# Performance work log

Hardware: AMD Instinct MI355X
Metric: run time of the kernel (lower is better)

## Reference

```python
import jax, jax.numpy as jnp
import numpy as np

B, C, Cs, CI, H, W = 4, 256, 256, 128, 64, 64

def setup_inputs() -> dict:
    key = jax.random.key(0)
    ks = jax.random.split(key, 9)
    sq = 1.0 / np.sqrt(C)
    ss = 1.0 / np.sqrt(Cs)
    return {
        "x_main": jax.random.normal(ks[0], (B, C, H, W), jnp.float32),
        "z_p": jax.random.normal(ks[1], (B, Cs, H, W), jnp.float32),
        "Wq": jax.random.normal(ks[2], (CI, C), jnp.float32) * sq,
        "bq": jax.random.normal(ks[3], (CI,), jnp.float32) * 0.01,
        "Wk": jax.random.normal(ks[4], (CI, Cs), jnp.float32) * ss,
        "bk": jax.random.normal(ks[5], (CI,), jnp.float32) * 0.01,
        "Wv": jax.random.normal(ks[6], (C, Cs), jnp.float32) * ss,
        "bv": jax.random.normal(ks[7], (C,), jnp.float32) * 0.01,
        "gamma": jax.random.normal(ks[8], (1,), jnp.float32) * 0.1,
    }

def reference(x_main, z_p, Wq, bq, Wk, bk, Wv, bv, gamma):
    b, c, h, w = x_main.shape
    n = h * w
    xm = x_main.reshape(b, c, n)          # [B, C, N]
    zf = z_p.reshape(b, z_p.shape[1], n)  # [B, Cs, M] (M == N here)
    # 1x1 convs == per-pixel channel projections
    q = jnp.einsum('oc,bcn->bon', Wq, xm) + bq[None, :, None]  # [B, CI, N]
    k = jnp.einsum('oc,bcm->bom', Wk, zf) + bk[None, :, None]  # [B, CI, M]
    v = jnp.einsum('oc,bcm->bom', Wv, zf) + bv[None, :, None]  # [B, C, M]
    # energy[b, n, m] = q_n . k_m  (no scaling, as in the original)
    energy = jnp.einsum('bcn,bcm->bnm', q, k)
    attention = jax.nn.softmax(energy, axis=-1)
    out = jnp.einsum('bom,bnm->bon', v, attention)  # [B, C, N]
    out = out.reshape(b, c, h, w)
    return gamma * out + x_main
```

## Files before the change

### kernel.cpp

```cpp
#include <hip/hip_runtime.h>
#include <hip/hip_bf16.h>


typedef __bf16  bf16x8  __attribute__((ext_vector_type(8)));
typedef float   f32x16  __attribute__((ext_vector_type(16)));

#define LOG2E 1.4426950408889634f

union BF8 { __hip_bfloat162 h[4]; bf16x8 v; };

__device__ inline bf16x8 pack8(const float f[8]) {
  BF8 u;
#pragma unroll
  for (int i = 0; i < 4; i++)
    u.h[i] = __float22bfloat162_rn(float2{f[2 * i], f[2 * i + 1]});
  return u.v;
}

__device__ inline void dma16(const void* g, void* l) {
  __builtin_amdgcn_global_load_lds(
      (const __attribute__((address_space(1))) unsigned int*)g,
      (__attribute__((address_space(3))) unsigned int*)l, 16, 0, 0);
}

__global__ __launch_bounds__(256, 2) void proj_mfma(
    const float* __restrict__ x, const float* __restrict__ z,
    const float* __restrict__ Wq, const float* __restrict__ bq,
    const float* __restrict__ Wk, const float* __restrict__ bk,
    const float* __restrict__ Wv, const float* __restrict__ bv,
    __hip_bfloat16* __restrict__ qp, __hip_bfloat16* __restrict__ kp,
    __hip_bfloat16* __restrict__ vp)
{
  extern __shared__ float xs[];
  const int bi = blockIdx.x;
  int mode, b, t, h = 0;
  if (bi < 512) { mode = bi >> 8; b = (bi & 255) >> 6; t = bi & 63; }
  else { int j = bi - 512; mode = 2; b = j >> 7; t = (j & 127) >> 1; h = j & 1; }
  const int n0 = t * 64;
  const float* X    = (mode == 0) ? x  : z;
  const float* W    = (mode == 0) ? Wq : (mode == 1) ? Wk : Wv;
  const float* bias = (mode == 0) ? bq : (mode == 1) ? bk : bv;

  const int tid = threadIdx.x;
  const int w = tid >> 6, lane = tid & 63, l32 = lane & 31, half = lane >> 5;

  {
    const float* gx = X + (size_t)b * (256 * 4096) + n0
                    + (size_t)(lane >> 4) * 4096 + (lane & 15) * 4;
#pragma unroll
    for (int it = 0; it < 16; it++) {
      int ch0 = w * 64 + it * 4;
      dma16(gx + (size_t)ch0 * 4096, xs + ch0 * 64 + lane * 4);
    }
  }

  const int obase = (mode == 2) ? 128 * h : 0;
  const int och = obase + w * 32 + l32;
  bf16x8 wf[16];
  {
    const float* wr = W + (size_t)och * 256 + half * 8;
#pragma unroll
    for (int cs = 0; cs < 16; cs++) {
      float f[8];
#pragma unroll
      for (int j = 0; j < 8; j++) f[j] = wr[cs * 16 + j];
      wf[cs] = pack8(f);
    }
  }
  __syncthreads();

  f32x16 O0, O1;
#pragma unroll
  for (int r = 0; r < 16; r++) { O0[r] = 0.f; O1[r] = 0.f; }

  const float* xc = xs + (half * 8) * 64 + l32;
  if (mode != 2) {
#pragma unroll
    for (int cs = 0; cs < 16; cs++) {
      float f0[8], f1[8];
#pragma unroll
      for (int j = 0; j < 8; j++) {
        f0[j] = xc[cs * 1024 + j * 64];
        f1[j] = xc[cs * 1024 + j * 64 + 32];
      }
      bf16x8 x0 = pack8(f0), x1 = pack8(f1);
      O0 = __builtin_amdgcn_mfma_f32_32x32x16_bf16(x0, wf[cs], O0, 0, 0, 0);
      O1 = __builtin_amdgcn_mfma_f32_32x32x16_bf16(x1, wf[cs], O1, 0, 0, 0);
    }
  } else {
#pragma unroll
    for (int cs = 0; cs < 16; cs++) {
      float f0[8], f1[8];
#pragma unroll
      for (int j = 0; j < 8; j++) {
        f0[j] = xc[cs * 1024 + j * 64];
        f1[j] = xc[cs * 1024 + j * 64 + 32];
      }
      bf16x8 x0 = pack8(f0), x1 = pack8(f1);
      O0 = __builtin_amdgcn_mfma_f32_32x32x16_bf16(wf[cs], x0, O0, 0, 0, 0);
      O1 = __builtin_amdgcn_mfma_f32_32x32x16_bf16(wf[cs], x1, O1, 0, 0, 0);
    }
  }

  if (mode == 0) {
    const float bb = bias[och];
    __hip_bfloat16* qb = qp + (size_t)(b * 4096 + n0) * 128 + och;
#pragma unroll
    for (int p = 0; p < 2; p++) {
      const f32x16& O = p ? O1 : O0;
#pragma unroll
      for (int r = 0; r < 16; r++) {
        int pix = p * 32 + (r & 3) + 8 * (r >> 2) + 4 * half;
        qb[(size_t)pix * 128] = __float2bfloat16((O[r] + bb) * LOG2E);
      }
    }
  } else if (mode == 1) {
    const float bb = bias[och];
    __hip_bfloat16* kb = kp + (size_t)(b * 128) * 4096
        + (och >> 4) * 512 + ((och >> 3) & 1) * 256 + (och & 7);
#pragma unroll
    for (int p = 0; p < 2; p++) {
      const f32x16& O = p ? O1 : O0;
#pragma unroll
      for (int r = 0; r < 16; r++) {
        int key = n0 + p * 32 + (r & 3) + 8 * (r >> 2) + 4 * half;
        kb[(size_t)(key >> 5) * 4096 + (key & 31) * 8] =
            __float2bfloat16(O[r] + bb);
      }
    }
  } else {
    float bvv[16];
#pragma unroll
    for (int r = 0; r < 16; r++)
      bvv[r] = bias[128 * h + 32 * w + (r & 3) + 8 * (r >> 2) + 4 * half];
    __hip_bfloat16* vb = vp + (size_t)(b * 128 + t * 2) * 8192
        + (4 * h + w) * 1024 + ((l32 >> 4) & 1) * 512 + ((l32 >> 3) & 1) * 256
        + (l32 & 7);
#pragma unroll
    for (int p = 0; p < 2; p++) {
      const f32x16& O = p ? O1 : O0;
#pragma unroll
      for (int r = 0; r < 16; r++) {
        int row = (r & 3) + 8 * (r >> 2) + 4 * half;
        vb[(size_t)p * 8192 + row * 8] = __float2bfloat16(O[r] + bvv[r]);
      }
    }
  }
}

struct AttnSmem {
  union {
    __hip_bfloat16 kbuf[2][8192];
    float ostage[256][33];
  } u;
  float redu[4][32];
  float rinv[32];
};

union U4 { unsigned u[4]; bf16x8 v; };

__global__ __launch_bounds__(256, 2) void attn_kernel(
    const __hip_bfloat16* __restrict__ qv, const __hip_bfloat16* __restrict__ kv,
    const __hip_bfloat16* __restrict__ vv,
    const float* __restrict__ x_main, const float* __restrict__ gammap,
    float* __restrict__ out)
{
  __shared__ AttnSmem sm;
  const int i  = blockIdx.x;
  const int b  = (i & 7) >> 1;
  const int qt = ((i >> 3) << 1) | (i & 1);
  const int n0 = qt * 32;
  const int tid  = threadIdx.x;
  const int w    = tid >> 6, lane = tid & 63, l32 = lane & 31, half = lane >> 5;
  const int kh   = w >> 1, chh = w & 1;

  bf16x8 qf[8];
  {
    const __hip_bfloat16* qb = qv + ((size_t)(b * 4096 + n0 + l32)) * 128 + half * 8;
#pragma unroll
    for (int cs = 0; cs < 8; cs++) qf[cs] = *(const bf16x8*)(qb + cs * 16);
  }

  const __hip_bfloat16* kg = kv + (size_t)(b * 128) * 4096;
  const __hip_bfloat16* vg = vv + (size_t)(b * 128) * 8192;

  auto stage = [&](int t) {
    __hip_bfloat16* kd = sm.u.kbuf[t & 1];
    const __hip_bfloat16* ksrc = kg + (size_t)t * 8192 + lane * 8;
#pragma unroll
    for (int c = 0; c < 4; c++) {
      int ck = w * 4 + c;
      dma16(ksrc + ck * 512, kd + ck * 512 + lane * 8);
    }
  };

  f32x16 Oacc[4];
#pragma unroll
  for (int c = 0; c < 4; c++)
#pragma unroll
    for (int r = 0; r < 16; r++) Oacc[c][r] = 0.f;

  float l_lane = 0.f;

  auto qk_tile = [&](int t) -> f32x16 {
    const __hip_bfloat16* kbase = sm.u.kbuf[t & 1] + kh * 4096 + lane * 8;
    f32x16 Sa, Sb;
#pragma unroll
    for (int r = 0; r < 16; r++) { Sa[r] = 0.f; Sb[r] = 0.f; }
#pragma unroll
    for (int cs = 0; cs < 4; cs++) {
      bf16x8 kf = *(const bf16x8*)(kbase + cs * 512);
      Sa = __builtin_amdgcn_mfma_f32_32x32x16_bf16(kf, qf[cs], Sa, 0, 0, 0);
    }
#pragma unroll
    for (int cs = 4; cs < 8; cs++) {
      bf16x8 kf = *(const bf16x8*)(kbase + cs * 512);
      Sb = __builtin_amdgcn_mfma_f32_32x32x16_bf16(kf, qf[cs], Sb, 0, 0, 0);
    }
    return Sa + Sb;
  };

  auto pv_tile = [&](int t, const f32x16& S) {
    unsigned p2[8];
    float lsub = 0.f;
#pragma unroll
    for (int t2 = 0; t2 < 8; t2++) {
      float a = exp2f(S[2 * t2]     - 64.0f);
      float c = exp2f(S[2 * t2 + 1] - 64.0f);
      lsub += a + c;
      union { __hip_bfloat162 h; unsigned u; } cv;
      cv.h = __float22bfloat162_rn(float2{a, c});
      p2[t2] = cv.u;
    }
    l_lane += lsub;
    unsigned r2[8];
#pragma unroll
    for (int t2 = 0; t2 < 8; t2++) r2[t2] = (unsigned)__shfl_xor((int)p2[t2], 32);
    U4 f0, f1;
    if (half == 0) {
      f0.u[0] = p2[0]; f0.u[1] = p2[1]; f0.u[2] = r2[0]; f0.u[3] = r2[1];
      f1.u[0] = p2[4]; f1.u[1] = p2[5]; f1.u[2] = r2[4]; f1.u[3] = r2[5];
    } else {
      f0.u[0] = r2[2]; f0.u[1] = r2[3]; f0.u[2] = p2[2]; f0.u[3] = p2[3];
      f1.u[0] = r2[6]; f1.u[1] = r2[7]; f1.u[2] = p2[6]; f1.u[3] = p2[7];
    }
    const bf16x8 pf0 = f0.v, pf1 = f1.v;
    const __hip_bfloat16* vb = vg + (size_t)(t * 2 + kh) * 8192
                             + chh * 4096 + lane * 8;
#pragma unroll
    for (int c = 0; c < 4; c++) {
      bf16x8 v0 = *(const bf16x8*)(vb + c * 1024);
      Oacc[c] = __builtin_amdgcn_mfma_f32_32x32x16_bf16(pf0, v0, Oacc[c], 0, 0, 0);
      bf16x8 v1 = *(const bf16x8*)(vb + c * 1024 + 512);
      Oacc[c] = __builtin_amdgcn_mfma_f32_32x32x16_bf16(pf1, v1, Oacc[c], 0, 0, 0);
    }
  };

  stage(0);
  __syncthreads();
  stage(1);
  {
    f32x16 S = qk_tile(0);
    pv_tile(0, S);
  }
#pragma unroll 1
  for (int t = 1; t < 64; ++t) {
    __syncthreads();
    if (t < 63) stage(t + 1);
    f32x16 S = qk_tile(t);
    pv_tile(t, S);
  }

  float lfull = l_lane + __shfl_xor(l_lane, 32);
  if (lane < 32) sm.redu[w][l32] = lfull;
  __syncthreads();
  if (kh == 0) {
#pragma unroll
    for (int c = 0; c < 4; c++) {
      int ch = (chh * 4 + c) * 32 + l32;
#pragma unroll
      for (int r = 0; r < 16; r++) {
        int q = (r & 3) + 8 * (r >> 2) + 4 * half;
        sm.u.ostage[ch][q] = Oacc[c][r];
      }
    }
  }
  if (tid < 32) sm.rinv[tid] = 1.0f / (sm.redu[0][tid] + sm.redu[2][tid]);
  __syncthreads();
  if (kh == 1) {
#pragma unroll
    for (int c = 0; c < 4; c++) {
      int ch = (chh * 4 + c) * 32 + l32;
#pragma unroll
      for (int r = 0; r < 16; r++) {
        int q = (r & 3) + 8 * (r >> 2) + 4 * half;
        sm.u.ostage[ch][q] += Oacc[c][r];
      }
    }
  }
  __syncthreads();

  const float gmm = gammap[0];
  const int pix = tid & 31;
  const float ri = sm.rinv[pix];
#pragma unroll
  for (int j = 0; j < 32; ++j) {
    int ch = (tid >> 5) * 32 + j;
    size_t g = ((size_t)(b * 256 + ch)) * 4096 + n0 + pix;
    out[g] = gmm * sm.u.ostage[ch][pix] * ri + x_main[g];
  }
}

extern "C" void kernel_launch(void* const* d_in, const int* in_sizes, int n_in,
                              void* d_out, int out_size, void* d_ws, size_t ws_size,
                              hipStream_t stream) {
  (void)in_sizes; (void)n_in; (void)out_size; (void)ws_size;
  const float* x  = (const float*)d_in[0];
  const float* z  = (const float*)d_in[1];
  const float* Wq = (const float*)d_in[2];
  const float* bq = (const float*)d_in[3];
  const float* Wk = (const float*)d_in[4];
  const float* bk = (const float*)d_in[5];
  const float* Wv = (const float*)d_in[6];
  const float* bv = (const float*)d_in[7];
  const float* gm = (const float*)d_in[8];
  float* out = (float*)d_out;

  char* ws = (char*)d_ws;
  const size_t QSZ = (size_t)4 * 4096 * 128 * sizeof(__hip_bfloat16);
  __hip_bfloat16* qp = (__hip_bfloat16*)(ws);
  __hip_bfloat16* kp = (__hip_bfloat16*)(ws + QSZ);
  __hip_bfloat16* vp = (__hip_bfloat16*)(ws + 2 * QSZ);

  const int proj_smem = 256 * 64 * sizeof(float);
  (void)hipFuncSetAttribute((const void*)proj_mfma,
                            hipFuncAttributeMaxDynamicSharedMemorySize,
                            proj_smem);

  proj_mfma<<<1024, 256, proj_smem, stream>>>(x, z, Wq, bq, Wk, bk, Wv, bv,
                                              qp, kp, vp);
  attn_kernel<<<512, 256, 0, stream>>>(qp, kp, vp, x, gm, out);
}
```

Before: 242.2 us.

## Pre-pack inputs and weights into MFMA fragment layout, drop attention shuffles

Adds a prep kernel that converts x, z and the three weight matrices to bf16 in MFMA-fragment-tiled layouts. The projection kernel then loads operands directly with vector loads and writes Q/K in a fragment layout, with a key permutation chosen so the attention kernel no longer needs cross-half shuffles to build P fragments. Attention also swaps operand order in PV, uses a single QK accumulator, and raises occupancy to 3 blocks. In exchange there is an extra kernel launch and an extra bf16 round trip of x and z through global memory.

```diff
diff --git a/kernel.cpp b/kernel.cpp
--- a/kernel.cpp
+++ b/kernel.cpp
@@ -8,6 +8,7 @@
 #define LOG2E 1.4426950408889634f
 
 union BF8 { __hip_bfloat162 h[4]; bf16x8 v; };
+union U4  { unsigned u[4]; bf16x8 v; };
 
 __device__ inline bf16x8 pack8(const float f[8]) {
   BF8 u;
@@ -23,126 +24,130 @@
       (__attribute__((address_space(3))) unsigned int*)l, 16, 0, 0);
 }
 
+__global__ __launch_bounds__(256) void prep_kernel(
+    const float* __restrict__ x, const float* __restrict__ z,
+    const float* __restrict__ Wq, const float* __restrict__ Wk,
+    const float* __restrict__ Wv,
+    __hip_bfloat16* __restrict__ xf, __hip_bfloat16* __restrict__ zf,
+    __hip_bfloat16* __restrict__ wfr)
+{
+  __shared__ float lds[256 * 65];
+  const int bi = blockIdx.x;
+  const int tid = threadIdx.x;
+  if (bi < 512) {
+    const int sel = bi >> 8;
+    const int b   = (bi >> 6) & 3;
+    const int pc  = bi & 63;
+    const float* in = sel ? z : x;
+    __hip_bfloat16* outp = sel ? zf : xf;
+    const size_t ib = (size_t)b * 256 * 4096 + pc * 64;
+#pragma unroll 4
+    for (int r = 0; r < 64; r++) {
+      int ch = r * 4 + (tid >> 6);
+      lds[ch * 65 + (tid & 63)] = in[ib + (size_t)ch * 4096 + (tid & 63)];
+    }
+    __syncthreads();
+    const size_t ob = ((size_t)(b * 128 + pc * 2)) * 8192;
+#pragma unroll
+    for (int i = 0; i < 8; i++) {
+      int c = i * 256 + tid;
+      int grp = c >> 10, cs = (c >> 6) & 15, rem = c & 63;
+      int hf = rem >> 5, l32 = rem & 31;
+      float f[8];
+      int chb = cs * 16 + hf * 8;
+#pragma unroll
+      for (int j = 0; j < 8; j++)
+        f[j] = lds[(chb + j) * 65 + grp * 32 + l32];
+      *(bf16x8*)(outp + ob + grp * 8192 + cs * 512 + hf * 256 + l32 * 8) =
+          pack8(f);
+    }
+  } else {
+    const int base = (bi - 512) * 4096;
+#pragma unroll
+    for (int i = 0; i < 16; i++) {
+      int c = base + i * 256 + tid;
+      const float* Ws; __hip_bfloat16* dst; int rc;
+      if (c < 4096)      { Ws = Wq; dst = wfr;          rc = c; }
+      else if (c < 8192) { Ws = Wk; dst = wfr + 32768;  rc = c - 4096; }
+      else               { Ws = Wv; dst = wfr + 65536;  rc = c - 8192; }
+      int ot = rc >> 10, cs = (rc >> 6) & 15, rem = rc & 63;
+      int hf = rem >> 5, l32 = rem & 31;
+      const float* src = Ws + (ot * 32 + l32) * 256 + cs * 16 + hf * 8;
+      float f[8];
+#pragma unroll
+      for (int j = 0; j < 8; j++) f[j] = src[j];
+      *(bf16x8*)(dst + ot * 8192 + cs * 512 + hf * 256 + l32 * 8) = pack8(f);
+    }
+  }
+}
+
 __global__ __launch_bounds__(256, 2) void proj_mfma(
-    const float* __restrict__ x, const float* __restrict__ z,
-    const float* __restrict__ Wq, const float* __restrict__ bq,
-    const float* __restrict__ Wk, const float* __restrict__ bk,
-    const float* __restrict__ Wv, const float* __restrict__ bv,
+    const __hip_bfloat16* __restrict__ xf, const __hip_bfloat16* __restrict__ zf,
+    const __hip_bfloat16* __restrict__ wfr,
+    const float* __restrict__ bq, const float* __restrict__ bk,
+    const float* __restrict__ bv,
     __hip_bfloat16* __restrict__ qp, __hip_bfloat16* __restrict__ kp,
     __hip_bfloat16* __restrict__ vp)
 {
-  extern __shared__ float xs[];
   const int bi = blockIdx.x;
-  int mode, b, t, h = 0;
-  if (bi < 512) { mode = bi >> 8; b = (bi & 255) >> 6; t = bi & 63; }
-  else { int j = bi - 512; mode = 2; b = j >> 7; t = (j & 127) >> 1; h = j & 1; }
-  const int n0 = t * 64;
-  const float* X    = (mode == 0) ? x  : z;
-  const float* W    = (mode == 0) ? Wq : (mode == 1) ? Wk : Wv;
+  int mode, b, pc, h = 0;
+  if (bi < 256) { mode = bi >> 7; b = (bi >> 5) & 3; pc = bi & 31; }
+  else { int j = bi - 256; mode = 2; b = j >> 6; pc = (j >> 1) & 31; h = j & 1; }
+  const int tid = threadIdx.x, w = tid >> 6, lane = tid & 63,
+            l32 = lane & 31, half = lane >> 5;
+
+  const __hip_bfloat16* X = (mode == 0) ? xf : zf;
+  const int wtile = (mode == 2 ? h * 4 : 0) + w;
+  const int wbase = (mode == 0) ? 0 : (mode == 1) ? 32768 : 65536;
+  const __hip_bfloat16* wp = wfr + wbase + wtile * 8192 + lane * 8;
+  bf16x8 wfg[16];
+#pragma unroll
+  for (int cs = 0; cs < 16; cs++) wfg[cs] = *(const bf16x8*)(wp + cs * 512);
+
   const float* bias = (mode == 0) ? bq : (mode == 1) ? bk : bv;
-
-  const int tid = threadIdx.x;
-  const int w = tid >> 6, lane = tid & 63, l32 = lane & 31, half = lane >> 5;
-
-  {
-    const float* gx = X + (size_t)b * (256 * 4096) + n0
-                    + (size_t)(lane >> 4) * 4096 + (lane & 15) * 4;
-#pragma unroll
-    for (int it = 0; it < 16; it++) {
-      int ch0 = w * 64 + it * 4;
-      dma16(gx + (size_t)ch0 * 4096, xs + ch0 * 64 + lane * 4);
-    }
-  }
-
-  const int obase = (mode == 2) ? 128 * h : 0;
-  const int och = obase + w * 32 + l32;
-  bf16x8 wf[16];
-  {
-    const float* wr = W + (size_t)och * 256 + half * 8;
+  const int ochb = (mode == 2 ? h * 128 : 0) + w * 32;
+  float bb[16];
+#pragma unroll
+  for (int r = 0; r < 16; r++)
+    bb[r] = bias[ochb + (r & 3) + 8 * (r >> 2) + 4 * half];
+
+  const int t4 = (l32 >> 2) & 3;
+  const int kperm = (t4 == 1 || t4 == 2) ? (l32 ^ 12) : l32;
+
+#pragma unroll 1
+  for (int it = 0; it < 4; it++) {
+    const int pg = pc * 4 + it;
+    const __hip_bfloat16* xb = X + ((size_t)(b * 128 + pg)) * 8192 + lane * 8;
+    f32x16 O = {};
 #pragma unroll
     for (int cs = 0; cs < 16; cs++) {
-      float f[8];
-#pragma unroll
-      for (int j = 0; j < 8; j++) f[j] = wr[cs * 16 + j];
-      wf[cs] = pack8(f);
-    }
-  }
-  __syncthreads();
-
-  f32x16 O0, O1;
-#pragma unroll
-  for (int r = 0; r < 16; r++) { O0[r] = 0.f; O1[r] = 0.f; }
-
-  const float* xc = xs + (half * 8) * 64 + l32;
-  if (mode != 2) {
-#pragma unroll
-    for (int cs = 0; cs < 16; cs++) {
-      float f0[8], f1[8];
-#pragma unroll
-      for (int j = 0; j < 8; j++) {
-        f0[j] = xc[cs * 1024 + j * 64];
-        f1[j] = xc[cs * 1024 + j * 64 + 32];
-      }
-      bf16x8 x0 = pack8(f0), x1 = pack8(f1);
-      O0 = __builtin_amdgcn_mfma_f32_32x32x16_bf16(x0, wf[cs], O0, 0, 0, 0);
-      O1 = __builtin_amdgcn_mfma_f32_32x32x16_bf16(x1, wf[cs], O1, 0, 0, 0);
-    }
-  } else {
-#pragma unroll
-    for (int cs = 0; cs < 16; cs++) {
-      float f0[8], f1[8];
-#pragma unroll
-      for (int j = 0; j < 8; j++) {
-        f0[j] = xc[cs * 1024 + j * 64];
-        f1[j] = xc[cs * 1024 + j * 64 + 32];
-      }
-      bf16x8 x0 = pack8(f0), x1 = pack8(f1);
-      O0 = __builtin_amdgcn_mfma_f32_32x32x16_bf16(wf[cs], x0, O0, 0, 0, 0);
-      O1 = __builtin_amdgcn_mfma_f32_32x32x16_bf16(wf[cs], x1, O1, 0, 0, 0);
-    }
-  }
-
-  if (mode == 0) {
-    const float bb = bias[och];
-    __hip_bfloat16* qb = qp + (size_t)(b * 4096 + n0) * 128 + och;
-#pragma unroll
-    for (int p = 0; p < 2; p++) {
-      const f32x16& O = p ? O1 : O0;
-#pragma unroll
-      for (int r = 0; r < 16; r++) {
-        int pix = p * 32 + (r & 3) + 8 * (r >> 2) + 4 * half;
-        qb[(size_t)pix * 128] = __float2bfloat16((O[r] + bb) * LOG2E);
-      }
-    }
-  } else if (mode == 1) {
-    const float bb = bias[och];
-    __hip_bfloat16* kb = kp + (size_t)(b * 128) * 4096
-        + (och >> 4) * 512 + ((och >> 3) & 1) * 256 + (och & 7);
-#pragma unroll
-    for (int p = 0; p < 2; p++) {
-      const f32x16& O = p ? O1 : O0;
-#pragma unroll
-      for (int r = 0; r < 16; r++) {
-        int key = n0 + p * 32 + (r & 3) + 8 * (r >> 2) + 4 * half;
-        kb[(size_t)(key >> 5) * 4096 + (key & 31) * 8] =
-            __float2bfloat16(O[r] + bb);
-      }
-    }
-  } else {
-    float bvv[16];
-#pragma unroll
-    for (int r = 0; r < 16; r++)
-      bvv[r] = bias[128 * h + 32 * w + (r & 3) + 8 * (r >> 2) + 4 * half];
-    __hip_bfloat16* vb = vp + (size_t)(b * 128 + t * 2) * 8192
-        + (4 * h + w) * 1024 + ((l32 >> 4) & 1) * 512 + ((l32 >> 3) & 1) * 256
-        + (l32 & 7);
-#pragma unroll
-    for (int p = 0; p < 2; p++) {
-      const f32x16& O = p ? O1 : O0;
-#pragma unroll
-      for (int r = 0; r < 16; r++) {
-        int row = (r & 3) + 8 * (r >> 2) + 4 * half;
-        vb[(size_t)p * 8192 + row * 8] = __float2bfloat16(O[r] + bvv[r]);
+      bf16x8 xr = *(const bf16x8*)(xb + cs * 512);
+      O = __builtin_amdgcn_mfma_f32_32x32x16_bf16(wfg[cs], xr, O, 0, 0, 0);
+    }
+    if (mode == 0) {
+      __hip_bfloat16* qb = qp + ((size_t)(b * 128 + pg)) * 4096;
+#pragma unroll
+      for (int r = 0; r < 16; r++) {
+        int oc = ochb + (r & 3) + 8 * (r >> 2) + 4 * half;
+        qb[(oc >> 4) * 512 + ((oc >> 3) & 1) * 256 + l32 * 8 + (oc & 7)] =
+            __float2bfloat16((O[r] + bb[r]) * LOG2E);
+      }
+    } else if (mode == 1) {
+      __hip_bfloat16* kb = kp + ((size_t)(b * 128 + pg)) * 4096;
+#pragma unroll
+      for (int r = 0; r < 16; r++) {
+        int oc = ochb + (r & 3) + 8 * (r >> 2) + 4 * half;
+        kb[(oc >> 4) * 512 + ((oc >> 3) & 1) * 256 + kperm * 8 + (oc & 7)] =
+            __float2bfloat16(O[r] + bb[r]);
+      }
+    } else {
+      __hip_bfloat16* vb = vp + ((size_t)(b * 128 + pg)) * 8192
+          + (h * 4 + w) * 1024 + (l32 >> 4) * 512 + ((l32 >> 3) & 1) * 256
+          + (l32 & 7);
+#pragma unroll
+      for (int r = 0; r < 16; r++) {
+        int rr = (r & 3) + 8 * (r >> 2) + 4 * half;
+        vb[rr * 8] = __float2bfloat16(O[r] + bb[r]);
       }
     }
   }
@@ -157,9 +162,7 @@
   float rinv[32];
 };
 
-union U4 { unsigned u[4]; bf16x8 v; };
-
-__global__ __launch_bounds__(256, 2) void attn_kernel(
+__global__ __launch_bounds__(256, 3) void attn_kernel(
     const __hip_bfloat16* __restrict__ qv, const __hip_bfloat16* __restrict__ kv,
     const __hip_bfloat16* __restrict__ vv,
     const float* __restrict__ x_main, const float* __restrict__ gammap,
@@ -171,14 +174,14 @@
   const int qt = ((i >> 3) << 1) | (i & 1);
   const int n0 = qt * 32;
   const int tid  = threadIdx.x;
-  const int w    = tid >> 6, lane = tid & 63, l32 = lane & 31, half = lane >> 5;
+  const int w    = tid >> 6, lane = tid & 63, l32 = lane & 31;
   const int kh   = w >> 1, chh = w & 1;
 
   bf16x8 qf[8];
   {
-    const __hip_bfloat16* qb = qv + ((size_t)(b * 4096 + n0 + l32)) * 128 + half * 8;
-#pragma unroll
-    for (int cs = 0; cs < 8; cs++) qf[cs] = *(const bf16x8*)(qb + cs * 16);
+    const __hip_bfloat16* qb = qv + ((size_t)(b * 128 + qt)) * 4096 + lane * 8;
+#pragma unroll
+    for (int cs = 0; cs < 8; cs++) qf[cs] = *(const bf16x8*)(qb + cs * 512);
   }
 
   const __hip_bfloat16* kg = kv + (size_t)(b * 128) * 4096;
@@ -204,55 +207,40 @@
 
   auto qk_tile = [&](int t) -> f32x16 {
     const __hip_bfloat16* kbase = sm.u.kbuf[t & 1] + kh * 4096 + lane * 8;
-    f32x16 Sa, Sb;
-#pragma unroll
-    for (int r = 0; r < 16; r++) { Sa[r] = 0.f; Sb[r] = 0.f; }
-#pragma unroll
-    for (int cs = 0; cs < 4; cs++) {
+    f32x16 S = {};
+#pragma unroll
+    for (int cs = 0; cs < 8; cs++) {
       bf16x8 kf = *(const bf16x8*)(kbase + cs * 512);
-      Sa = __builtin_amdgcn_mfma_f32_32x32x16_bf16(kf, qf[cs], Sa, 0, 0, 0);
-    }
-#pragma unroll
-    for (int cs = 4; cs < 8; cs++) {
-      bf16x8 kf = *(const bf16x8*)(kbase + cs * 512);
-      Sb = __builtin_amdgcn_mfma_f32_32x32x16_bf16(kf, qf[cs], Sb, 0, 0, 0);
-    }
-    return Sa + Sb;
+      S = __builtin_amdgcn_mfma_f32_32x32x16_bf16(kf, qf[cs], S, 0, 0, 0);
+    }
+    return S;
   };
 
   auto pv_tile = [&](int t, const f32x16& S) {
     unsigned p2[8];
-    float lsub = 0.f;
-#pragma unroll
-    for (int t2 = 0; t2 < 8; t2++) {
-      float a = exp2f(S[2 * t2]     - 64.0f);
-      float c = exp2f(S[2 * t2 + 1] - 64.0f);
-      lsub += a + c;
+    float s0 = 0.f, s1 = 0.f;
+#pragma unroll
+    for (int i2 = 0; i2 < 8; i2++) {
+      float a = exp2f(S[2 * i2]     - 64.0f);
+      float c = exp2f(S[2 * i2 + 1] - 64.0f);
+      if (i2 & 1) s1 += a + c; else s0 += a + c;
       union { __hip_bfloat162 h; unsigned u; } cv;
       cv.h = __float22bfloat162_rn(float2{a, c});
-      p2[t2] = cv.u;
-    }
-    l_lane += lsub;
-    unsigned r2[8];
-#pragma unroll
-    for (int t2 = 0; t2 < 8; t2++) r2[t2] = (unsigned)__shfl_xor((int)p2[t2], 32);
+      p2[i2] = cv.u;
+    }
+    l_lane += s0 + s1;
     U4 f0, f1;
-    if (half == 0) {
-      f0.u[0] = p2[0]; f0.u[1] = p2[1]; f0.u[2] = r2[0]; f0.u[3] = r2[1];
-      f1.u[0] = p2[4]; f1.u[1] = p2[5]; f1.u[2] = r2[4]; f1.u[3] = r2[5];
-    } else {
-      f0.u[0] = r2[2]; f0.u[1] = r2[3]; f0.u[2] = p2[2]; f0.u[3] = p2[3];
-      f1.u[0] = r2[6]; f1.u[1] = r2[7]; f1.u[2] = p2[6]; f1.u[3] = p2[7];
-    }
+    f0.u[0] = p2[0]; f0.u[1] = p2[1]; f0.u[2] = p2[2]; f0.u[3] = p2[3];
+    f1.u[0] = p2[4]; f1.u[1] = p2[5]; f1.u[2] = p2[6]; f1.u[3] = p2[7];
     const bf16x8 pf0 = f0.v, pf1 = f1.v;
     const __hip_bfloat16* vb = vg + (size_t)(t * 2 + kh) * 8192
                              + chh * 4096 + lane * 8;
 #pragma unroll
     for (int c = 0; c < 4; c++) {
       bf16x8 v0 = *(const bf16x8*)(vb + c * 1024);
-      Oacc[c] = __builtin_amdgcn_mfma_f32_32x32x16_bf16(pf0, v0, Oacc[c], 0, 0, 0);
+      Oacc[c] = __builtin_amdgcn_mfma_f32_32x32x16_bf16(v0, pf0, Oacc[c], 0, 0, 0);
       bf16x8 v1 = *(const bf16x8*)(vb + c * 1024 + 512);
-      Oacc[c] = __builtin_amdgcn_mfma_f32_32x32x16_bf16(pf1, v1, Oacc[c], 0, 0, 0);
+      Oacc[c] = __builtin_amdgcn_mfma_f32_32x32x16_bf16(v1, pf1, Oacc[c], 0, 0, 0);
     }
   };
 
@@ -274,14 +262,14 @@
   float lfull = l_lane + __shfl_xor(l_lane, 32);
   if (lane < 32) sm.redu[w][l32] = lfull;
   __syncthreads();
+  const int hb = lane >> 5;
   if (kh == 0) {
 #pragma unroll
     for (int c = 0; c < 4; c++) {
-      int ch = (chh * 4 + c) * 32 + l32;
-#pragma unroll
-      for (int r = 0; r < 16; r++) {
-        int q = (r & 3) + 8 * (r >> 2) + 4 * half;
-        sm.u.ostage[ch][q] = Oacc[c][r];
+#pragma unroll
+      for (int r = 0; r < 16; r++) {
+        int ch = (chh * 4 + c) * 32 + (r & 3) + 8 * (r >> 2) + 4 * hb;
+        sm.u.ostage[ch][l32] = Oacc[c][r];
       }
     }
   }
@@ -290,11 +278,10 @@
   if (kh == 1) {
 #pragma unroll
     for (int c = 0; c < 4; c++) {
-      int ch = (chh * 4 + c) * 32 + l32;
-#pragma unroll
-      for (int r = 0; r < 16; r++) {
-        int q = (r & 3) + 8 * (r >> 2) + 4 * half;
-        sm.u.ostage[ch][q] += Oacc[c][r];
+#pragma unroll
+      for (int r = 0; r < 16; r++) {
+        int ch = (chh * 4 + c) * 32 + (r & 3) + 8 * (r >> 2) + 4 * hb;
+        sm.u.ostage[ch][l32] += Oacc[c][r];
       }
     }
   }
@@ -327,17 +314,15 @@
   float* out = (float*)d_out;
 
   char* ws = (char*)d_ws;
-  const size_t QSZ = (size_t)4 * 4096 * 128 * sizeof(__hip_bfloat16);
-  __hip_bfloat16* qp = (__hip_bfloat16*)(ws);
-  __hip_bfloat16* kp = (__hip_bfloat16*)(ws + QSZ);
-  __hip_bfloat16* vp = (__hip_bfloat16*)(ws + 2 * QSZ);
-
-  const int proj_smem = 256 * 64 * sizeof(float);
-  (void)hipFuncSetAttribute((const void*)proj_mfma,
-                            hipFuncAttributeMaxDynamicSharedMemorySize,
-                            proj_smem);
-
-  proj_mfma<<<1024, 256, proj_smem, stream>>>(x, z, Wq, bq, Wk, bk, Wv, bv,
-                                              qp, kp, vp);
+  const size_t MB = 1024 * 1024;
+  __hip_bfloat16* qp  = (__hip_bfloat16*)(ws);
+  __hip_bfloat16* kp  = (__hip_bfloat16*)(ws + 4 * MB);
+  __hip_bfloat16* vp  = (__hip_bfloat16*)(ws + 8 * MB);
+  __hip_bfloat16* xfp = (__hip_bfloat16*)(ws + 16 * MB);
+  __hip_bfloat16* zfp = (__hip_bfloat16*)(ws + 24 * MB);
+  __hip_bfloat16* wfp = (__hip_bfloat16*)(ws + 32 * MB);
+
+  prep_kernel<<<516, 256, 0, stream>>>(x, z, Wq, Wk, Wv, xfp, zfp, wfp);
+  proj_mfma  <<<512, 256, 0, stream>>>(xfp, zfp, wfp, bq, bk, bv, qp, kp, vp);
   attn_kernel<<<512, 256, 0, stream>>>(qp, kp, vp, x, gm, out);
 }
```

After: 215.4 us. -11.1%, faster.
